# Kernel tuning notes

Hardware: AMD Instinct MI355X
Metric: run time of the kernel (lower is better)

The kernel has to match this reference:

```python
import jax, jax.numpy as jnp
import numpy as np

N_ATOMS = 131072
N_TYPES = 256
D_IN = 64
D_OUT = 64


def setup_inputs() -> dict:
    key = jax.random.key(0)
    k_x, k_t, k_w, k_b = jax.random.split(key, 4)
    x = jax.random.normal(k_x, (N_ATOMS, D_IN), dtype=jnp.float32)
    atom_types = jax.random.randint(k_t, (N_ATOMS,), 0, N_TYPES, dtype=jnp.int64)
    # Per-atom-type linear weights/biases (the 'unique' table gathered per atom).
    W = jax.random.normal(k_w, (N_TYPES, D_OUT, D_IN), dtype=jnp.float32) * (1.0 / np.sqrt(D_IN))
    b = jax.random.normal(k_b, (N_TYPES, D_OUT), dtype=jnp.float32) * 0.01
    return {"x": x, "atom_types": atom_types, "W": W, "b": b}


def reference(x, atom_types, W, b):
    # Gather type-specific linear params per atom (gather_unique_first semantics),
    # apply the per-atom linear, then tanh.
    Wg = W[atom_types]          # [N, d_out, d_in]
    bg = b[atom_types]          # [N, d_out]
    y = jnp.einsum('noi,ni->no', Wg, x) + bg  # [N, d_out]
    return jnp.tanh(y)
```

## Files before the change

kernel.cpp:

```cpp
#include <hip/hip_runtime.h>

#define N_ATOMS 131072
#define N_TYPES 256
#define D 64
#define CAP 1024
#define BPT 4

using sfrag = __attribute__((ext_vector_type(8))) short;
using ffrag = __attribute__((ext_vector_type(4))) float;

__device__ __forceinline__ short f2bf(float f)
{
    union { float f; unsigned u; } v; v.f = f;
    unsigned r = v.u + 0x7FFFu + ((v.u >> 16) & 1u);
    return (short)(r >> 16);
}

__device__ __forceinline__ float fast_tanh(float v)
{
    float e = __expf(2.0f * v);
    return 1.0f - __fdividef(2.0f, e + 1.0f);
}

__global__ __launch_bounds__(256) void scatter_kernel(
    const int* __restrict__ types, int* __restrict__ cursor, int* __restrict__ bucket)
{
    __shared__ int lhist[N_TYPES];
    __shared__ int lbase[N_TYPES];
    __shared__ int lcur[N_TYPES];
    const int tid  = threadIdx.x;
    const int base = blockIdx.x * 1024;
    lhist[tid] = 0;
    __syncthreads();

    int ty[4];
#pragma unroll
    for (int k = 0; k < 4; ++k) ty[k] = types[base + k * 256 + tid];
#pragma unroll
    for (int k = 0; k < 4; ++k) atomicAdd(&lhist[ty[k]], 1);
    __syncthreads();

    const int cnt = lhist[tid];
    if (cnt > 0) lbase[tid] = atomicAdd(&cursor[tid], cnt);
    lcur[tid] = 0;
    __syncthreads();

#pragma unroll
    for (int k = 0; k < 4; ++k) {
        const int t = ty[k];
        const int p = atomicAdd(&lcur[t], 1);
        const int q = lbase[t] + p;
        if (q < CAP) bucket[t * CAP + q] = base + k * 256 + tid;
    }
}

__global__ __launch_bounds__(256, 4) void apply_kernel(
    const float* __restrict__ x, const float* __restrict__ W,
    const float* __restrict__ b, const int* __restrict__ bucket,
    const int* __restrict__ cursor, float* __restrict__ out)
{
    const int t = blockIdx.x & 255;
    const int j = blockIdx.x >> 8;
    int n = cursor[t];
    if (n > CAP) n = CAP;

    const int wave = threadIdx.x >> 6;
    const int lane = threadIdx.x & 63;
    const int c = lane & 15;
    const int q = lane >> 4;

    const int*   bk = bucket + (size_t)t * CAP;
    const float* Wt = W + (size_t)t * (D * D);

    const int stride = BPT * 4;
    int g = j * 4 + wave;
    if (g * 16 >= n) return;

    int aidx;
    {
        int ridx = g * 16 + c;
        if (ridx >= n) ridx = n - 1;
        aidx = bk[ridx];
    }

    sfrag Bf[4][2];
#pragma unroll
    for (int nt = 0; nt < 4; ++nt) {
#pragma unroll
        for (int ks = 0; ks < 2; ++ks) {
            const float4* wr = (const float4*)(Wt + (size_t)(nt * 16 + c) * D + ks * 32 + q * 8);
            float4 w0 = wr[0], w1 = wr[1];
            sfrag f;
            f[0] = f2bf(w0.x); f[1] = f2bf(w0.y); f[2] = f2bf(w0.z); f[3] = f2bf(w0.w);
            f[4] = f2bf(w1.x); f[5] = f2bf(w1.y); f[6] = f2bf(w1.z); f[7] = f2bf(w1.w);
            Bf[nt][ks] = f;
        }
    }
    float bias[4];
#pragma unroll
    for (int nt = 0; nt < 4; ++nt) bias[nt] = b[(size_t)t * D + nt * 16 + c];

    float4 x0, x1, x2, x3;
    {
        const float4* xr = (const float4*)x + (size_t)aidx * 16 + q * 2;
        x0 = xr[0]; x1 = xr[1]; x2 = xr[8]; x3 = xr[9];
    }

    while (true) {
        const int gn = g + stride;
        const bool more = (gn * 16 < n);

        int naidx = 0; float4 nx0, nx1, nx2, nx3;
        if (more) {
            int ridx = gn * 16 + c;
            if (ridx >= n) ridx = n - 1;
            naidx = bk[ridx];
            const float4* xr = (const float4*)x + (size_t)naidx * 16 + q * 2;
            nx0 = xr[0]; nx1 = xr[1]; nx2 = xr[8]; nx3 = xr[9];
        }

        sfrag A0, A1;
        A0[0] = f2bf(x0.x); A0[1] = f2bf(x0.y); A0[2] = f2bf(x0.z); A0[3] = f2bf(x0.w);
        A0[4] = f2bf(x1.x); A0[5] = f2bf(x1.y); A0[6] = f2bf(x1.z); A0[7] = f2bf(x1.w);
        A1[0] = f2bf(x2.x); A1[1] = f2bf(x2.y); A1[2] = f2bf(x2.z); A1[3] = f2bf(x2.w);
        A1[4] = f2bf(x3.x); A1[5] = f2bf(x3.y); A1[6] = f2bf(x3.z); A1[7] = f2bf(x3.w);

        const int base = g * 16;
        int  oat[4]; bool ov[4];
#pragma unroll
        for (int r = 0; r < 4; ++r) {
            ov[r]  = (base + q * 4 + r) < n;
            oat[r] = __shfl(aidx, q * 4 + r, 64);
        }

#pragma unroll
        for (int nt = 0; nt < 4; ++nt) {
            ffrag acc = {0.f, 0.f, 0.f, 0.f};
            acc = __builtin_amdgcn_mfma_f32_16x16x32_bf16(A0, Bf[nt][0], acc, 0, 0, 0);
            acc = __builtin_amdgcn_mfma_f32_16x16x32_bf16(A1, Bf[nt][1], acc, 0, 0, 0);
#pragma unroll
            for (int r = 0; r < 4; ++r) {
                if (ov[r])
                    out[(size_t)oat[r] * D + nt * 16 + c] = fast_tanh(acc[r] + bias[nt]);
            }
        }

        if (!more) break;
        g = gn; aidx = naidx;
        x0 = nx0; x1 = nx1; x2 = nx2; x3 = nx3;
    }
}

extern "C" void kernel_launch(void* const* d_in, const int* in_sizes, int n_in,
                              void* d_out, int out_size, void* d_ws, size_t ws_size,
                              hipStream_t stream)
{
    const float* x     = (const float*)d_in[0];
    const int*   types = (const int*)  d_in[1];
    const float* W     = (const float*)d_in[2];
    const float* b     = (const float*)d_in[3];
    float*       out   = (float*)d_out;

    int* cursor = (int*)d_ws;
    int* bucket = (int*)((char*)d_ws + 1024);

    hipMemsetAsync(cursor, 0, N_TYPES * sizeof(int), stream);
    scatter_kernel<<<dim3(N_ATOMS / 1024), dim3(256), 0, stream>>>(types, cursor, bucket);
    apply_kernel<<<dim3(BPT * N_TYPES), dim3(256), 0, stream>>>(x, W, b, bucket, cursor, out);
}
```

Before: 106.2 us.

## Fuse bucketing and per-type apply into one kernel with per-block type scan

Replaces the memset, global scatter kernel and apply kernel with a single kernel of one 1024-thread block per atom type. Each block scans the whole types array, collects the matching atom indices into a shared-memory queue, then runs the MFMA apply over them. This removes two launches and the global atomics/bucket traffic. In exchange every block reads all the types (256x redundant reads, mostly served from L2), and the number of blocks drops to 256. Atom order within a type becomes nondeterministic, but each atom is still written exactly once.

```diff
diff --git a/kernel.cpp b/kernel.cpp
--- a/kernel.cpp
+++ b/kernel.cpp
@@ -4,7 +4,6 @@
 #define N_TYPES 256
 #define D 64
 #define CAP 1024
-#define BPT 4
 
 using sfrag = __attribute__((ext_vector_type(8))) short;
 using ffrag = __attribute__((ext_vector_type(4))) float;
@@ -22,66 +21,24 @@
     return 1.0f - __fdividef(2.0f, e + 1.0f);
 }
 
-__global__ __launch_bounds__(256) void scatter_kernel(
-    const int* __restrict__ types, int* __restrict__ cursor, int* __restrict__ bucket)
+__global__ __launch_bounds__(1024, 4) void fused_kernel(
+    const float* __restrict__ x, const int* __restrict__ types,
+    const float* __restrict__ W, const float* __restrict__ b,
+    float* __restrict__ out)
 {
-    __shared__ int lhist[N_TYPES];
-    __shared__ int lbase[N_TYPES];
-    __shared__ int lcur[N_TYPES];
-    const int tid  = threadIdx.x;
-    const int base = blockIdx.x * 1024;
-    lhist[tid] = 0;
+    __shared__ int queue[CAP];
+    __shared__ int qcnt;
+
+    const int t   = blockIdx.x;
+    const int tid = threadIdx.x;
+    if (tid == 0) qcnt = 0;
     __syncthreads();
 
-    int ty[4];
-#pragma unroll
-    for (int k = 0; k < 4; ++k) ty[k] = types[base + k * 256 + tid];
-#pragma unroll
-    for (int k = 0; k < 4; ++k) atomicAdd(&lhist[ty[k]], 1);
-    __syncthreads();
-
-    const int cnt = lhist[tid];
-    if (cnt > 0) lbase[tid] = atomicAdd(&cursor[tid], cnt);
-    lcur[tid] = 0;
-    __syncthreads();
-
-#pragma unroll
-    for (int k = 0; k < 4; ++k) {
-        const int t = ty[k];
-        const int p = atomicAdd(&lcur[t], 1);
-        const int q = lbase[t] + p;
-        if (q < CAP) bucket[t * CAP + q] = base + k * 256 + tid;
-    }
-}
-
-__global__ __launch_bounds__(256, 4) void apply_kernel(
-    const float* __restrict__ x, const float* __restrict__ W,
-    const float* __restrict__ b, const int* __restrict__ bucket,
-    const int* __restrict__ cursor, float* __restrict__ out)
-{
-    const int t = blockIdx.x & 255;
-    const int j = blockIdx.x >> 8;
-    int n = cursor[t];
-    if (n > CAP) n = CAP;
-
-    const int wave = threadIdx.x >> 6;
-    const int lane = threadIdx.x & 63;
+    const int wave = tid >> 6;
+    const int lane = tid & 63;
     const int c = lane & 15;
     const int q = lane >> 4;
-
-    const int*   bk = bucket + (size_t)t * CAP;
     const float* Wt = W + (size_t)t * (D * D);
-
-    const int stride = BPT * 4;
-    int g = j * 4 + wave;
-    if (g * 16 >= n) return;
-
-    int aidx;
-    {
-        int ridx = g * 16 + c;
-        if (ridx >= n) ridx = n - 1;
-        aidx = bk[ridx];
-    }
 
     sfrag Bf[4][2];
 #pragma unroll
@@ -100,6 +57,32 @@
 #pragma unroll
     for (int nt = 0; nt < 4; ++nt) bias[nt] = b[(size_t)t * D + nt * 16 + c];
 
+    {
+        const int4* ty4 = (const int4*)types;
+#pragma unroll 4
+        for (int k = 0; k < 32; ++k) {
+            const int idx4 = k * 1024 + tid;
+            int4 tv = ty4[idx4];
+            const int a0 = idx4 * 4;
+            if (tv.x == t) { int p = atomicAdd(&qcnt, 1); if (p < CAP) queue[p] = a0;     }
+            if (tv.y == t) { int p = atomicAdd(&qcnt, 1); if (p < CAP) queue[p] = a0 + 1; }
+            if (tv.z == t) { int p = atomicAdd(&qcnt, 1); if (p < CAP) queue[p] = a0 + 2; }
+            if (tv.w == t) { int p = atomicAdd(&qcnt, 1); if (p < CAP) queue[p] = a0 + 3; }
+        }
+    }
+    __syncthreads();
+    int n = qcnt;
+    if (n > CAP) n = CAP;
+
+    int g = wave;
+    if (g * 16 >= n) return;
+
+    int aidx;
+    {
+        int ridx = g * 16 + c;
+        if (ridx >= n) ridx = n - 1;
+        aidx = queue[ridx];
+    }
     float4 x0, x1, x2, x3;
     {
         const float4* xr = (const float4*)x + (size_t)aidx * 16 + q * 2;
@@ -107,14 +90,14 @@
     }
 
     while (true) {
-        const int gn = g + stride;
+        const int gn = g + 16;
         const bool more = (gn * 16 < n);
 
         int naidx = 0; float4 nx0, nx1, nx2, nx3;
         if (more) {
             int ridx = gn * 16 + c;
             if (ridx >= n) ridx = n - 1;
-            naidx = bk[ridx];
+            naidx = queue[ridx];
             const float4* xr = (const float4*)x + (size_t)naidx * 16 + q * 2;
             nx0 = xr[0]; nx1 = xr[1]; nx2 = xr[8]; nx3 = xr[9];
         }
@@ -161,10 +144,5 @@
     const float* b     = (const float*)d_in[3];
     float*       out   = (float*)d_out;
 
-    int* cursor = (int*)d_ws;
-    int* bucket = (int*)((char*)d_ws + 1024);
-
-    hipMemsetAsync(cursor, 0, N_TYPES * sizeof(int), stream);
-    scatter_kernel<<<dim3(N_ATOMS / 1024), dim3(256), 0, stream>>>(types, cursor, bucket);
-    apply_kernel<<<dim3(BPT * N_TYPES), dim3(256), 0, stream>>>(x, W, b, bucket, cursor, out);
+    fused_kernel<<<dim3(N_TYPES), dim3(1024), 0, stream>>>(x, types, W, b, out);
 }
```

Result: slower. 110.8 us (+4.3%).

## Double blocks per type and drop register prefetch in favor of occupancy

Applied to the files above, without the earlier changes.

Doubles blocks per atom type from 4 to 8 and raises the launch-bounds occupancy hint from 4 to 8 blocks per CU. The software prefetch of the next group's x rows is removed, which frees registers so more waves can hide latency. The bucket index load is issued before the cursor read so the two overlap. Out-of-range bucket entries are clamped to index 0 rather than n-1, which relies on the bucket slots being readable even past the count.

```diff
diff --git a/kernel.cpp b/kernel.cpp
--- a/kernel.cpp
+++ b/kernel.cpp
@@ -4,7 +4,7 @@
 #define N_TYPES 256
 #define D 64
 #define CAP 1024
-#define BPT 4
+#define BPT 8
 
 using sfrag = __attribute__((ext_vector_type(8))) short;
 using ffrag = __attribute__((ext_vector_type(4))) float;
@@ -54,15 +54,13 @@
     }
 }
 
-__global__ __launch_bounds__(256, 4) void apply_kernel(
+__global__ __launch_bounds__(256, 8) void apply_kernel(
     const float* __restrict__ x, const float* __restrict__ W,
     const float* __restrict__ b, const int* __restrict__ bucket,
     const int* __restrict__ cursor, float* __restrict__ out)
 {
     const int t = blockIdx.x & 255;
     const int j = blockIdx.x >> 8;
-    int n = cursor[t];
-    if (n > CAP) n = CAP;
 
     const int wave = threadIdx.x >> 6;
     const int lane = threadIdx.x & 63;
@@ -72,16 +70,12 @@
     const int*   bk = bucket + (size_t)t * CAP;
     const float* Wt = W + (size_t)t * (D * D);
 
-    const int stride = BPT * 4;
     int g = j * 4 + wave;
-    if (g * 16 >= n) return;
 
-    int aidx;
-    {
-        int ridx = g * 16 + c;
-        if (ridx >= n) ridx = n - 1;
-        aidx = bk[ridx];
-    }
+    int raw = bk[g * 16 + c];
+
+    int n = cursor[t];
+    if (n > CAP) n = CAP;
 
     sfrag Bf[4][2];
 #pragma unroll
@@ -100,24 +94,13 @@
 #pragma unroll
     for (int nt = 0; nt < 4; ++nt) bias[nt] = b[(size_t)t * D + nt * 16 + c];
 
-    float4 x0, x1, x2, x3;
-    {
-        const float4* xr = (const float4*)x + (size_t)aidx * 16 + q * 2;
-        x0 = xr[0]; x1 = xr[1]; x2 = xr[8]; x3 = xr[9];
-    }
+    if (g * 16 >= n) return;
 
     while (true) {
-        const int gn = g + stride;
-        const bool more = (gn * 16 < n);
+        int aidx = ((unsigned)raw >= (unsigned)N_ATOMS) ? 0 : raw;
 
-        int naidx = 0; float4 nx0, nx1, nx2, nx3;
-        if (more) {
-            int ridx = gn * 16 + c;
-            if (ridx >= n) ridx = n - 1;
-            naidx = bk[ridx];
-            const float4* xr = (const float4*)x + (size_t)naidx * 16 + q * 2;
-            nx0 = xr[0]; nx1 = xr[1]; nx2 = xr[8]; nx3 = xr[9];
-        }
+        const float4* xr = (const float4*)x + (size_t)aidx * 16 + q * 2;
+        float4 x0 = xr[0], x1 = xr[1], x2 = xr[8], x3 = xr[9];
 
         sfrag A0, A1;
         A0[0] = f2bf(x0.x); A0[1] = f2bf(x0.y); A0[2] = f2bf(x0.z); A0[3] = f2bf(x0.w);
@@ -145,9 +128,9 @@
             }
         }
 
-        if (!more) break;
-        g = gn; aidx = naidx;
-        x0 = nx0; x1 = nx1; x2 = nx2; x3 = nx3;
+        g += 4 * BPT;
+        if (g * 16 >= n) break;
+        raw = bk[g * 16 + c];
     }
 }
 
```

New measurement: 129.3 us. 21.7% more time.
